# Performance work log

Measured on AMD Instinct MI355X. Metric: run time of the kernel, lower is better.

## Reference

```python
import jax, jax.numpy as jnp
import numpy as np

N = 100000
E = 300000
IN_C = 256
HID = 256   # 2 * out_channels
OUT_C = 128


def setup_inputs() -> dict:
    key = jax.random.key(0)
    k1, k2, k3, k4, k5 = jax.random.split(key, 5)
    x = jax.random.normal(k1, (N, IN_C), dtype=jnp.float32)
    edge_index = jax.random.randint(k2, (2, E), 0, N, dtype=jnp.int64)
    # Glorot-style init scale for GEMM weights
    W1 = jax.random.normal(k3, (IN_C, HID), dtype=jnp.float32) * (1.0 / np.sqrt(IN_C))
    b1 = jnp.zeros((HID,), dtype=jnp.float32)
    W2 = jax.random.normal(k4, (HID, OUT_C), dtype=jnp.float32) * (1.0 / np.sqrt(HID))
    b2 = jnp.zeros((OUT_C,), dtype=jnp.float32)
    return {"x": x, "edge_index": edge_index, "W1": W1, "b1": b1, "W2": W2, "b2": b2}


def _gcn_conv(x, W, b, src, dst, norm, n_nodes):
    # x: [N, Fin] -> transform then gather-scale-scatter aggregate
    h = x @ W                                   # [N, Fout]
    msgs = h[src] * norm[:, None]               # [E+N, Fout] (includes self-loops)
    out = jax.ops.segment_sum(msgs, dst, num_segments=n_nodes)
    return out + b


def _gcn_norm(edge_index, n_nodes):
    # add self-loops, compute symmetric deg^-1/2 normalization (PyG GCNConv default)
    loops = jnp.arange(n_nodes, dtype=edge_index.dtype)
    src = jnp.concatenate([edge_index[0], loops])
    dst = jnp.concatenate([edge_index[1], loops])
    deg = jax.ops.segment_sum(jnp.ones_like(dst, dtype=jnp.float32), dst, num_segments=n_nodes)
    dinv = jnp.where(deg > 0, jax.lax.rsqrt(deg), 0.0)
    norm = dinv[src] * dinv[dst]                # [E+N]
    return src, dst, norm


def reference(x, edge_index, W1, b1, W2, b2):
    n_nodes = x.shape[0]
    src, dst, norm = _gcn_norm(edge_index, n_nodes)
    h = _gcn_conv(x, W1, b1, src, dst, norm, n_nodes)
    h = jax.nn.relu(h)
    # dropout is identity in eval mode (reference baseline runs deterministic eval)
    return _gcn_conv(h, W2, b2, src, dst, norm, n_nodes)
```

## Files before the change

### kernel.cpp

```cpp
#include <hip/hip_runtime.h>
#include <stdint.h>

#define IN_C  256
#define HID   256
#define OUT_C 128
#define SCAN_BS 1024

typedef __bf16 bf16x8 __attribute__((ext_vector_type(8)));
typedef float  f32x4  __attribute__((ext_vector_type(4)));
typedef unsigned short u16x8 __attribute__((ext_vector_type(8)));
typedef unsigned short u16x4 __attribute__((ext_vector_type(4)));
typedef unsigned short u16x2 __attribute__((ext_vector_type(2)));

static __device__ __forceinline__ unsigned short f2b(float f) {
    union { float f; uint32_t u; } v; v.f = f;
    uint32_t r = v.u + 0x7fffu + ((v.u >> 16) & 1u);
    return (unsigned short)(r >> 16);
}
static __device__ __forceinline__ float b2f(unsigned short b) {
    union { uint32_t u; float f; } v; v.u = ((uint32_t)b) << 16;
    return v.f;
}

__global__ void k_zero_i(int* __restrict__ p, int n) {
    int i = blockIdx.x * blockDim.x + threadIdx.x;
    if (i < n) p[i] = 0;
}

__global__ void k_count(const int* __restrict__ dst, int* __restrict__ cnt, int e) {
    int i = blockIdx.x * blockDim.x + threadIdx.x;
    if (i < e) atomicAdd(&cnt[dst[i]], 1);
}

__global__ __launch_bounds__(SCAN_BS) void k_scan_block(
    const int* __restrict__ cnt, int* __restrict__ rs, int* __restrict__ bsum, int n) {
    __shared__ int s[SCAN_BS];
    const int tid = threadIdx.x;
    const int i = blockIdx.x * SCAN_BS + tid;
    int v = (i < n) ? cnt[i] + 1 : 0;
    s[tid] = v;
    __syncthreads();
    for (int off = 1; off < SCAN_BS; off <<= 1) {
        int t = (tid >= off) ? s[tid - off] : 0;
        __syncthreads();
        s[tid] += t;
        __syncthreads();
    }
    if (i < n) rs[i] = s[tid] - v;
    if (tid == SCAN_BS - 1) bsum[blockIdx.x] = s[tid];
}

__global__ void k_scan_sums(int* __restrict__ bsum, int nb) {
    __shared__ int s[128];
    const int tid = threadIdx.x;
    int v = (tid < nb) ? bsum[tid] : 0;
    s[tid] = v;
    __syncthreads();
    for (int off = 1; off < 128; off <<= 1) {
        int t = (tid >= off) ? s[tid - off] : 0;
        __syncthreads();
        s[tid] += t;
        __syncthreads();
    }
    if (tid < nb) bsum[tid] = s[tid] - v;
}

__global__ void k_scan_add(int* __restrict__ rs, int* __restrict__ cur,
                           const int* __restrict__ bsum, const int* __restrict__ cnt,
                           float* __restrict__ dinv, int2* __restrict__ csrw, int n) {
    int i = blockIdx.x * blockDim.x + threadIdx.x;
    if (i < n) {
        int v = rs[i] + bsum[i >> 10];
        rs[i] = v;
        cur[i] = v + 1;
        float dp1 = (float)(cnt[i] + 1);
        dinv[i] = rsqrtf(dp1);
        csrw[v] = make_int2(i, __float_as_int(1.0f / dp1));
    }
}

__global__ void k_fill(const int* __restrict__ src, const int* __restrict__ dst,
                       const float* __restrict__ dinv,
                       int* __restrict__ cur, int2* __restrict__ csrw, int e) {
    int i = blockIdx.x * blockDim.x + threadIdx.x;
    if (i < e) {
        int s = src[i], d = dst[i];
        int p = atomicAdd(&cur[d], 1);
        csrw[p] = make_int2(s, __float_as_int(dinv[s] * dinv[d]));
    }
}

__global__ void k_prep(const float* __restrict__ W1, const float* __restrict__ W2,
                       unsigned short* __restrict__ W1T, unsigned short* __restrict__ W2T) {
    int i = blockIdx.x * blockDim.x + threadIdx.x;
    if (i < 65536) W1T[i] = f2b(W1[(i & 255) * HID + (i >> 8)]);
    if (i < 32768) W2T[i] = f2b(W2[(i & 255) * OUT_C + (i >> 8)]);
}

__global__ __launch_bounds__(512) void k_gemm1(
    const float* __restrict__ x, const unsigned short* __restrict__ W1T,
    unsigned short* __restrict__ t1, int n) {
    __shared__ __align__(16) unsigned short As[128 * 64];
    __shared__ __align__(16) unsigned short Bs[256 * 64];
    const int tid  = threadIdx.x;
    const int row0 = blockIdx.x * 128;
    const int wid = tid >> 6, lane = tid & 63;
    const int wm = wid >> 2, wn = wid & 3;
    const int lrow = lane & 15, lgrp = lane >> 4;

    f32x4 acc[4][4];
    #pragma unroll
    for (int i = 0; i < 4; ++i)
        #pragma unroll
        for (int j = 0; j < 4; ++j)
            acc[i][j] = (f32x4){0.f, 0.f, 0.f, 0.f};

    for (int kt = 0; kt < 4; ++kt) {
        #pragma unroll
        for (int i = 0; i < 2; ++i) {
            int chunk = tid + 512 * i;
            int r = chunk >> 3, c = chunk & 7;
            int grow = row0 + r;
            u16x8 pk = {0, 0, 0, 0, 0, 0, 0, 0};
            if (grow < n) {
                const float* sp = x + (size_t)grow * IN_C + kt * 64 + c * 8;
                float4 a = *(const float4*)sp;
                float4 b = *(const float4*)(sp + 4);
                pk[0] = f2b(a.x); pk[1] = f2b(a.y); pk[2] = f2b(a.z); pk[3] = f2b(a.w);
                pk[4] = f2b(b.x); pk[5] = f2b(b.y); pk[6] = f2b(b.z); pk[7] = f2b(b.w);
            }
            *(u16x8*)&As[r * 64 + ((c ^ (r & 7)) * 8)] = pk;
        }
        #pragma unroll
        for (int i = 0; i < 4; ++i) {
            int chunk = tid + 512 * i;
            int nn = chunk >> 3, c = chunk & 7;
            u16x8 pk = *(const u16x8*)&W1T[(size_t)nn * 256 + kt * 64 + c * 8];
            *(u16x8*)&Bs[nn * 64 + ((c ^ (nn & 7)) * 8)] = pk;
        }
        __syncthreads();
        #pragma unroll
        for (int kk = 0; kk < 2; ++kk) {
            const int cfrag = kk * 4 + lgrp;
            bf16x8 av[4], bv[4];
            #pragma unroll
            for (int mf = 0; mf < 4; ++mf) {
                int r = wm * 64 + mf * 16 + lrow;
                av[mf] = *(const bf16x8*)&As[r * 64 + ((cfrag ^ (r & 7)) * 8)];
            }
            #pragma unroll
            for (int nf = 0; nf < 4; ++nf) {
                int cc = wn * 64 + nf * 16 + lrow;
                bv[nf] = *(const bf16x8*)&Bs[cc * 64 + ((cfrag ^ (cc & 7)) * 8)];
            }
            #pragma unroll
            for (int mf = 0; mf < 4; ++mf)
                #pragma unroll
                for (int nf = 0; nf < 4; ++nf)
                    acc[mf][nf] = __builtin_amdgcn_mfma_f32_16x16x32_bf16(
                        av[mf], bv[nf], acc[mf][nf], 0, 0, 0);
        }
        __syncthreads();
    }
    #pragma unroll
    for (int mf = 0; mf < 4; ++mf)
        #pragma unroll
        for (int j = 0; j < 4; ++j) {
            int grow = row0 + wm * 64 + mf * 16 + lgrp * 4 + j;
            if (grow < n) {
                #pragma unroll
                for (int nf = 0; nf < 4; ++nf) {
                    int col = wn * 64 + nf * 16 + lrow;
                    t1[(size_t)grow * HID + col] = f2b(acc[mf][nf][j]);
                }
            }
        }
}

__global__ __launch_bounds__(256) void k_agg1(
    const unsigned short* __restrict__ t1, const int* __restrict__ rs,
    const int* __restrict__ cnt, const int2* __restrict__ csrw,
    const float* __restrict__ b1, unsigned short* __restrict__ out1, int n) {
    const int w = blockIdx.x * 4 + (threadIdx.x >> 6);
    const int nodeA = w * 2, nodeB = w * 2 + 1;
    if (nodeA >= n) return;
    const bool hasB = (nodeB < n);
    const int lane = threadIdx.x & 63;
    const int ch = lane * 4;
    const int begA = rs[nodeA], mA = cnt[nodeA] + 1;
    int begB = 0, mB = 0;
    if (hasB) { begB = rs[nodeB]; mB = cnt[nodeB] + 1; }
    float a0 = 0.f, a1 = 0.f, a2 = 0.f, a3 = 0.f;
    float c0 = 0.f, c1 = 0.f, c2 = 0.f, c3 = 0.f;
    const int mmax = mA > mB ? mA : mB;
    for (int j = 0; j < mmax; ++j) {
        if (j < mA) {
            int2 p = csrw[begA + j];
            float wA = __int_as_float(p.y);
            u16x4 u = *(const u16x4*)&t1[(size_t)p.x * HID + ch];
            a0 += b2f(u[0]) * wA; a1 += b2f(u[1]) * wA;
            a2 += b2f(u[2]) * wA; a3 += b2f(u[3]) * wA;
        }
        if (j < mB) {
            int2 p = csrw[begB + j];
            float wB = __int_as_float(p.y);
            u16x4 u = *(const u16x4*)&t1[(size_t)p.x * HID + ch];
            c0 += b2f(u[0]) * wB; c1 += b2f(u[1]) * wB;
            c2 += b2f(u[2]) * wB; c3 += b2f(u[3]) * wB;
        }
    }
    float4 bb = *(const float4*)(b1 + ch);
    u16x4 o;
    o[0] = f2b(fmaxf(a0 + bb.x, 0.f));
    o[1] = f2b(fmaxf(a1 + bb.y, 0.f));
    o[2] = f2b(fmaxf(a2 + bb.z, 0.f));
    o[3] = f2b(fmaxf(a3 + bb.w, 0.f));
    *(u16x4*)&out1[(size_t)nodeA * HID + ch] = o;
    if (hasB) {
        u16x4 q;
        q[0] = f2b(fmaxf(c0 + bb.x, 0.f));
        q[1] = f2b(fmaxf(c1 + bb.y, 0.f));
        q[2] = f2b(fmaxf(c2 + bb.z, 0.f));
        q[3] = f2b(fmaxf(c3 + bb.w, 0.f));
        *(u16x4*)&out1[(size_t)nodeB * HID + ch] = q;
    }
}

__global__ __launch_bounds__(256) void k_gemm2(
    const unsigned short* __restrict__ out1, const unsigned short* __restrict__ W2T,
    unsigned short* __restrict__ t2, int n) {
    __shared__ __align__(16) unsigned short As[128 * 64];
    __shared__ __align__(16) unsigned short Bs[128 * 64];
    const int tid  = threadIdx.x;
    const int row0 = blockIdx.x * 128;
    const int wid = tid >> 6, lane = tid & 63;
    const int wm = wid >> 1, wn = wid & 1;
    const int lrow = lane & 15, lgrp = lane >> 4;

    f32x4 acc[4][4];
    #pragma unroll
    for (int i = 0; i < 4; ++i)
        #pragma unroll
        for (int j = 0; j < 4; ++j)
            acc[i][j] = (f32x4){0.f, 0.f, 0.f, 0.f};

    for (int kt = 0; kt < 4; ++kt) {
        #pragma unroll
        for (int i = 0; i < 4; ++i) {
            int chunk = tid + 256 * i;
            int r = chunk >> 3, c = chunk & 7;
            int grow = row0 + r;
            u16x8 pk = {0, 0, 0, 0, 0, 0, 0, 0};
            if (grow < n)
                pk = *(const u16x8*)&out1[(size_t)grow * HID + kt * 64 + c * 8];
            *(u16x8*)&As[r * 64 + ((c ^ (r & 7)) * 8)] = pk;
        }
        #pragma unroll
        for (int i = 0; i < 4; ++i) {
            int chunk = tid + 256 * i;
            int nn = chunk >> 3, c = chunk & 7;
            u16x8 pk = *(const u16x8*)&W2T[(size_t)nn * 256 + kt * 64 + c * 8];
            *(u16x8*)&Bs[nn * 64 + ((c ^ (nn & 7)) * 8)] = pk;
        }
        __syncthreads();
        #pragma unroll
        for (int kk = 0; kk < 2; ++kk) {
            const int cfrag = kk * 4 + lgrp;
            bf16x8 av[4], bv[4];
            #pragma unroll
            for (int mf = 0; mf < 4; ++mf) {
                int r = wm * 64 + mf * 16 + lrow;
                av[mf] = *(const bf16x8*)&As[r * 64 + ((cfrag ^ (r & 7)) * 8)];
            }
            #pragma unroll
            for (int nf = 0; nf < 4; ++nf) {
                int cc = wn * 64 + nf * 16 + lrow;
                bv[nf] = *(const bf16x8*)&Bs[cc * 64 + ((cfrag ^ (cc & 7)) * 8)];
            }
            #pragma unroll
            for (int mf = 0; mf < 4; ++mf)
                #pragma unroll
                for (int nf = 0; nf < 4; ++nf)
                    acc[mf][nf] = __builtin_amdgcn_mfma_f32_16x16x32_bf16(
                        av[mf], bv[nf], acc[mf][nf], 0, 0, 0);
        }
        __syncthreads();
    }
    #pragma unroll
    for (int mf = 0; mf < 4; ++mf)
        #pragma unroll
        for (int j = 0; j < 4; ++j) {
            int grow = row0 + wm * 64 + mf * 16 + lgrp * 4 + j;
            if (grow < n) {
                #pragma unroll
                for (int nf = 0; nf < 4; ++nf) {
                    int col = wn * 64 + nf * 16 + lrow;
                    t2[(size_t)grow * OUT_C + col] = f2b(acc[mf][nf][j]);
                }
            }
        }
}

__global__ __launch_bounds__(256) void k_agg2(
    const unsigned short* __restrict__ t2, const int* __restrict__ rs,
    const int* __restrict__ cnt, const int2* __restrict__ csrw,
    const float* __restrict__ b2, float* __restrict__ out, int n) {
    const int w = blockIdx.x * 4 + (threadIdx.x >> 6);
    const int nodeA = w * 2, nodeB = w * 2 + 1;
    if (nodeA >= n) return;
    const bool hasB = (nodeB < n);
    const int lane = threadIdx.x & 63;
    const int ch = lane * 2;
    const int begA = rs[nodeA], mA = cnt[nodeA] + 1;
    int begB = 0, mB = 0;
    if (hasB) { begB = rs[nodeB]; mB = cnt[nodeB] + 1; }
    float a0 = 0.f, a1 = 0.f, c0 = 0.f, c1 = 0.f;
    const int mmax = mA > mB ? mA : mB;
    for (int j = 0; j < mmax; ++j) {
        if (j < mA) {
            int2 p = csrw[begA + j];
            float wA = __int_as_float(p.y);
            u16x2 u = *(const u16x2*)&t2[(size_t)p.x * OUT_C + ch];
            a0 += b2f(u[0]) * wA; a1 += b2f(u[1]) * wA;
        }
        if (j < mB) {
            int2 p = csrw[begB + j];
            float wB = __int_as_float(p.y);
            u16x2 u = *(const u16x2*)&t2[(size_t)p.x * OUT_C + ch];
            c0 += b2f(u[0]) * wB; c1 += b2f(u[1]) * wB;
        }
    }
    float2 bb = *(const float2*)(b2 + ch);
    *(float2*)&out[(size_t)nodeA * OUT_C + ch] = make_float2(a0 + bb.x, a1 + bb.y);
    if (hasB)
        *(float2*)&out[(size_t)nodeB * OUT_C + ch] = make_float2(c0 + bb.x, c1 + bb.y);
}

extern "C" void kernel_launch(void* const* d_in, const int* in_sizes, int n_in,
                              void* d_out, int out_size, void* d_ws, size_t ws_size,
                              hipStream_t stream) {
    const float* x  = (const float*)d_in[0];
    const int*   ei = (const int*)d_in[1];
    const float* W1 = (const float*)d_in[2];
    const float* b1 = (const float*)d_in[3];
    const float* W2 = (const float*)d_in[4];
    const float* b2 = (const float*)d_in[5];
    float* out = (float*)d_out;

    const int n = in_sizes[0] / IN_C;
    const int e = in_sizes[1] / 2;
    const int* src = ei;
    const int* dst = ei + e;

    int*   cnt  = (int*)d_ws;
    int*   rs   = cnt + n;
    int*   cur  = rs + n;
    int*   bsum = cur + n;
    float* dinv = (float*)(bsum + 128);
    int2*  csrw = (int2*)(dinv + n);
    unsigned short* W1T = (unsigned short*)(csrw + (size_t)e + n);
    unsigned short* W2T = W1T + 65536;
    unsigned short* t1  = W2T + 32768;
    unsigned short* out1 = t1 + (size_t)n * HID;
    unsigned short* t2  = t1;

    const int nb = (n + SCAN_BS - 1) / SCAN_BS;

    k_zero_i<<<(n + 255) / 256, 256, 0, stream>>>(cnt, n);
    k_count<<<(e + 255) / 256, 256, 0, stream>>>(dst, cnt, e);
    k_scan_block<<<nb, SCAN_BS, 0, stream>>>(cnt, rs, bsum, n);
    k_scan_sums<<<1, 128, 0, stream>>>(bsum, nb);
    k_scan_add<<<(n + 255) / 256, 256, 0, stream>>>(rs, cur, bsum, cnt, dinv, csrw, n);
    k_fill<<<(e + 255) / 256, 256, 0, stream>>>(src, dst, dinv, cur, csrw, e);
    k_prep<<<256, 256, 0, stream>>>(W1, W2, W1T, W2T);

    const int mb = (n + 127) / 128;
    k_gemm1<<<mb, 512, 0, stream>>>(x, W1T, t1, n);
    const int aggblk = (n + 7) / 8;
    k_agg1<<<aggblk, 256, 0, stream>>>(t1, rs, cnt, csrw, b1, out1, n);
    k_gemm2<<<mb, 256, 0, stream>>>(out1, W2T, t2, n);
    k_agg2<<<aggblk, 256, 0, stream>>>(t2, rs, cnt, csrw, b2, out, n);
}
```

Before: 213.8 us.

## Load GEMM tiles directly to LDS and split first GEMM across columns

Both dense GEMMs now stage their tiles with global_load_lds, which copies global memory straight into LDS and skips the register round trip. The K tile shrinks to 32 and the first GEMM keeps x as fp32 in LDS, converting to bf16 with v_cvt_pk_bf16_f32 only when building fragments. The first GEMM is also split into two column blocks of 256 threads, so each x row tile is fetched by two blocks and has to rely on cache to avoid the extra traffic. The change also doubles the number of barrier iterations and uses unswizzled B and A tiles in the second GEMM, which may cause LDS bank conflicts.

```diff
diff --git a/kernel.cpp b/kernel.cpp
--- a/kernel.cpp
+++ b/kernel.cpp
@@ -11,6 +11,7 @@
 typedef unsigned short u16x8 __attribute__((ext_vector_type(8)));
 typedef unsigned short u16x4 __attribute__((ext_vector_type(4)));
 typedef unsigned short u16x2 __attribute__((ext_vector_type(2)));
+typedef unsigned int u32;
 
 static __device__ __forceinline__ unsigned short f2b(float f) {
     union { float f; uint32_t u; } v; v.f = f;
@@ -20,6 +21,17 @@
 static __device__ __forceinline__ float b2f(unsigned short b) {
     union { uint32_t u; float f; } v; v.u = ((uint32_t)b) << 16;
     return v.f;
+}
+
+typedef __attribute__((address_space(1))) const u32 gas_u32;
+typedef __attribute__((address_space(3))) u32 las_u32;
+static __device__ __forceinline__ void gld16(const void* g, void* l) {
+    __builtin_amdgcn_global_load_lds((gas_u32*)g, (las_u32*)l, 16, 0, 0);
+}
+static __device__ __forceinline__ u32 cvtpk(float lo, float hi) {
+    u32 r;
+    asm("v_cvt_pk_bf16_f32 %0, %1, %2" : "=v"(r) : "v"(lo), "v"(hi));
+    return r;
 }
 
 __global__ void k_zero_i(int* __restrict__ p, int n) {
@@ -97,15 +109,16 @@
     if (i < 32768) W2T[i] = f2b(W2[(i & 255) * OUT_C + (i >> 8)]);
 }
 
-__global__ __launch_bounds__(512) void k_gemm1(
+__global__ __launch_bounds__(256) void k_gemm1(
     const float* __restrict__ x, const unsigned short* __restrict__ W1T,
     unsigned short* __restrict__ t1, int n) {
-    __shared__ __align__(16) unsigned short As[128 * 64];
-    __shared__ __align__(16) unsigned short Bs[256 * 64];
-    const int tid  = threadIdx.x;
-    const int row0 = blockIdx.x * 128;
+    __shared__ __align__(16) float Af[128 * 32];
+    __shared__ __align__(16) unsigned short Bs[128 * 32];
+    const int tid = threadIdx.x;
+    const int bm = blockIdx.x >> 1, bn = blockIdx.x & 1;
+    const int row0 = bm * 128, col0 = bn * 128;
     const int wid = tid >> 6, lane = tid & 63;
-    const int wm = wid >> 2, wn = wid & 3;
+    const int wm = wid >> 1, wn = wid & 1;
     const int lrow = lane & 15, lgrp = lane >> 4;
 
     f32x4 acc[4][4];
@@ -115,51 +128,44 @@
         for (int j = 0; j < 4; ++j)
             acc[i][j] = (f32x4){0.f, 0.f, 0.f, 0.f};
 
-    for (int kt = 0; kt < 4; ++kt) {
+    for (int kt = 0; kt < 8; ++kt) {
+        #pragma unroll
+        for (int i = 0; i < 4; ++i) {
+            int s = tid + 256 * i;
+            int r = s >> 3, c = s & 7;
+            int grow = row0 + r; if (grow > n - 1) grow = n - 1;
+            gld16(x + (size_t)grow * IN_C + kt * 32 + ((c ^ (r & 7)) << 2), Af + s * 4);
+        }
         #pragma unroll
         for (int i = 0; i < 2; ++i) {
-            int chunk = tid + 512 * i;
-            int r = chunk >> 3, c = chunk & 7;
-            int grow = row0 + r;
-            u16x8 pk = {0, 0, 0, 0, 0, 0, 0, 0};
-            if (grow < n) {
-                const float* sp = x + (size_t)grow * IN_C + kt * 64 + c * 8;
-                float4 a = *(const float4*)sp;
-                float4 b = *(const float4*)(sp + 4);
-                pk[0] = f2b(a.x); pk[1] = f2b(a.y); pk[2] = f2b(a.z); pk[3] = f2b(a.w);
-                pk[4] = f2b(b.x); pk[5] = f2b(b.y); pk[6] = f2b(b.z); pk[7] = f2b(b.w);
-            }
-            *(u16x8*)&As[r * 64 + ((c ^ (r & 7)) * 8)] = pk;
-        }
-        #pragma unroll
-        for (int i = 0; i < 4; ++i) {
-            int chunk = tid + 512 * i;
-            int nn = chunk >> 3, c = chunk & 7;
-            u16x8 pk = *(const u16x8*)&W1T[(size_t)nn * 256 + kt * 64 + c * 8];
-            *(u16x8*)&Bs[nn * 64 + ((c ^ (nn & 7)) * 8)] = pk;
-        }
-        __syncthreads();
-        #pragma unroll
-        for (int kk = 0; kk < 2; ++kk) {
-            const int cfrag = kk * 4 + lgrp;
-            bf16x8 av[4], bv[4];
+            int s = tid + 256 * i;
+            int nn = s >> 2, c = s & 3;
+            gld16(W1T + (size_t)(col0 + nn) * 256 + kt * 32 + c * 8, Bs + s * 8);
+        }
+        __syncthreads();
+
+        bf16x8 av[4], bv[4];
+        #pragma unroll
+        for (int mf = 0; mf < 4; ++mf) {
+            int r = wm * 64 + mf * 16 + lrow;
+            f32x4 l = *(const f32x4*)&Af[r * 32 + (((2 * lgrp) ^ (r & 7)) << 2)];
+            f32x4 h = *(const f32x4*)&Af[r * 32 + (((2 * lgrp + 1) ^ (r & 7)) << 2)];
+            union { u32 w[4]; bf16x8 b; } u;
+            u.w[0] = cvtpk(l[0], l[1]); u.w[1] = cvtpk(l[2], l[3]);
+            u.w[2] = cvtpk(h[0], h[1]); u.w[3] = cvtpk(h[2], h[3]);
+            av[mf] = u.b;
+        }
+        #pragma unroll
+        for (int nf = 0; nf < 4; ++nf) {
+            int cc = wn * 64 + nf * 16 + lrow;
+            bv[nf] = *(const bf16x8*)&Bs[cc * 32 + lgrp * 8];
+        }
+        #pragma unroll
+        for (int mf = 0; mf < 4; ++mf)
             #pragma unroll
-            for (int mf = 0; mf < 4; ++mf) {
-                int r = wm * 64 + mf * 16 + lrow;
-                av[mf] = *(const bf16x8*)&As[r * 64 + ((cfrag ^ (r & 7)) * 8)];
-            }
-            #pragma unroll
-            for (int nf = 0; nf < 4; ++nf) {
-                int cc = wn * 64 + nf * 16 + lrow;
-                bv[nf] = *(const bf16x8*)&Bs[cc * 64 + ((cfrag ^ (cc & 7)) * 8)];
-            }
-            #pragma unroll
-            for (int mf = 0; mf < 4; ++mf)
-                #pragma unroll
-                for (int nf = 0; nf < 4; ++nf)
-                    acc[mf][nf] = __builtin_amdgcn_mfma_f32_16x16x32_bf16(
-                        av[mf], bv[nf], acc[mf][nf], 0, 0, 0);
-        }
+            for (int nf = 0; nf < 4; ++nf)
+                acc[mf][nf] = __builtin_amdgcn_mfma_f32_16x16x32_bf16(
+                    av[mf], bv[nf], acc[mf][nf], 0, 0, 0);
         __syncthreads();
     }
     #pragma unroll
@@ -170,7 +176,7 @@
             if (grow < n) {
                 #pragma unroll
                 for (int nf = 0; nf < 4; ++nf) {
-                    int col = wn * 64 + nf * 16 + lrow;
+                    int col = col0 + wn * 64 + nf * 16 + lrow;
                     t1[(size_t)grow * HID + col] = f2b(acc[mf][nf][j]);
                 }
             }
@@ -229,9 +235,9 @@
 __global__ __launch_bounds__(256) void k_gemm2(
     const unsigned short* __restrict__ out1, const unsigned short* __restrict__ W2T,
     unsigned short* __restrict__ t2, int n) {
-    __shared__ __align__(16) unsigned short As[128 * 64];
-    __shared__ __align__(16) unsigned short Bs[128 * 64];
-    const int tid  = threadIdx.x;
+    __shared__ __align__(16) unsigned short Ah[128 * 32];
+    __shared__ __align__(16) unsigned short Bs[128 * 32];
+    const int tid = threadIdx.x;
     const int row0 = blockIdx.x * 128;
     const int wid = tid >> 6, lane = tid & 63;
     const int wm = wid >> 1, wn = wid & 1;
@@ -244,46 +250,39 @@
         for (int j = 0; j < 4; ++j)
             acc[i][j] = (f32x4){0.f, 0.f, 0.f, 0.f};
 
-    for (int kt = 0; kt < 4; ++kt) {
-        #pragma unroll
-        for (int i = 0; i < 4; ++i) {
-            int chunk = tid + 256 * i;
-            int r = chunk >> 3, c = chunk & 7;
-            int grow = row0 + r;
-            u16x8 pk = {0, 0, 0, 0, 0, 0, 0, 0};
-            if (grow < n)
-                pk = *(const u16x8*)&out1[(size_t)grow * HID + kt * 64 + c * 8];
-            *(u16x8*)&As[r * 64 + ((c ^ (r & 7)) * 8)] = pk;
-        }
-        #pragma unroll
-        for (int i = 0; i < 4; ++i) {
-            int chunk = tid + 256 * i;
-            int nn = chunk >> 3, c = chunk & 7;
-            u16x8 pk = *(const u16x8*)&W2T[(size_t)nn * 256 + kt * 64 + c * 8];
-            *(u16x8*)&Bs[nn * 64 + ((c ^ (nn & 7)) * 8)] = pk;
-        }
-        __syncthreads();
-        #pragma unroll
-        for (int kk = 0; kk < 2; ++kk) {
-            const int cfrag = kk * 4 + lgrp;
-            bf16x8 av[4], bv[4];
+    for (int kt = 0; kt < 8; ++kt) {
+        #pragma unroll
+        for (int i = 0; i < 2; ++i) {
+            int s = tid + 256 * i;
+            int r = s >> 2, c = s & 3;
+            int grow = row0 + r; if (grow > n - 1) grow = n - 1;
+            gld16(out1 + (size_t)grow * HID + kt * 32 + c * 8, Ah + s * 8);
+        }
+        #pragma unroll
+        for (int i = 0; i < 2; ++i) {
+            int s = tid + 256 * i;
+            int nn = s >> 2, c = s & 3;
+            gld16(W2T + (size_t)nn * 256 + kt * 32 + c * 8, Bs + s * 8);
+        }
+        __syncthreads();
+
+        bf16x8 av[4], bv[4];
+        #pragma unroll
+        for (int mf = 0; mf < 4; ++mf) {
+            int r = wm * 64 + mf * 16 + lrow;
+            av[mf] = *(const bf16x8*)&Ah[r * 32 + lgrp * 8];
+        }
+        #pragma unroll
+        for (int nf = 0; nf < 4; ++nf) {
+            int cc = wn * 64 + nf * 16 + lrow;
+            bv[nf] = *(const bf16x8*)&Bs[cc * 32 + lgrp * 8];
+        }
+        #pragma unroll
+        for (int mf = 0; mf < 4; ++mf)
             #pragma unroll
-            for (int mf = 0; mf < 4; ++mf) {
-                int r = wm * 64 + mf * 16 + lrow;
-                av[mf] = *(const bf16x8*)&As[r * 64 + ((cfrag ^ (r & 7)) * 8)];
-            }
-            #pragma unroll
-            for (int nf = 0; nf < 4; ++nf) {
-                int cc = wn * 64 + nf * 16 + lrow;
-                bv[nf] = *(const bf16x8*)&Bs[cc * 64 + ((cfrag ^ (cc & 7)) * 8)];
-            }
-            #pragma unroll
-            for (int mf = 0; mf < 4; ++mf)
-                #pragma unroll
-                for (int nf = 0; nf < 4; ++nf)
-                    acc[mf][nf] = __builtin_amdgcn_mfma_f32_16x16x32_bf16(
-                        av[mf], bv[nf], acc[mf][nf], 0, 0, 0);
-        }
+            for (int nf = 0; nf < 4; ++nf)
+                acc[mf][nf] = __builtin_amdgcn_mfma_f32_16x16x32_bf16(
+                    av[mf], bv[nf], acc[mf][nf], 0, 0, 0);
         __syncthreads();
     }
     #pragma unroll
@@ -375,7 +374,7 @@
     k_prep<<<256, 256, 0, stream>>>(W1, W2, W1T, W2T);
 
     const int mb = (n + 127) / 128;
-    k_gemm1<<<mb, 512, 0, stream>>>(x, W1T, t1, n);
+    k_gemm1<<<mb * 2, 256, 0, stream>>>(x, W1T, t1, n);
     const int aggblk = (n + 7) / 8;
     k_agg1<<<aggblk, 256, 0, stream>>>(t1, rs, cnt, csrw, b1, out1, n);
     k_gemm2<<<mb, 256, 0, stream>>>(out1, W2T, t2, n);
```

After: 216.9 us. About the same (+1.4%).
